# Performance work log

Measured on AMD Instinct MI355X. Metric: run time of the kernel, lower is better.

Reference implementation:

```python
import jax, jax.numpy as jnp
import numpy as np

EMBED = 768
HEAD = 256

def setup_inputs() -> dict:
    key = jax.random.key(0)
    k1, k2, k3, k4 = jax.random.split(key, 4)
    res_stream = jax.random.normal(k1, (512, 128, EMBED), dtype=jnp.float32)
    # torch Linear(embed, head, bias=False): y = x @ W.T, W: [head, embed].
    # Store as [embed, head] so y = x @ W.
    Wk = jax.random.normal(k2, (EMBED, HEAD), dtype=jnp.float32) * (EMBED ** -0.5)
    Wq = jax.random.normal(k3, (EMBED, HEAD), dtype=jnp.float32) * (EMBED ** -0.5)
    Wv = jax.random.normal(k4, (EMBED, HEAD), dtype=jnp.float32) * (EMBED ** -0.5)
    return {"res_stream": res_stream, "Wk": Wk, "Wq": Wq, "Wv": Wv}

def reference(res_stream, Wk, Wq, Wv):
    B, T, E = res_stream.shape
    q = jnp.einsum('bte,eh->bth', res_stream, Wq)  # [B,T,H]
    k = jnp.einsum('bte,eh->bth', res_stream, Wk)
    v = jnp.einsum('bte,eh->bth', res_stream, Wv)
    # NOTE: original scales by embed**-0.5 (not head_size**-0.5)
    scores = jnp.einsum('bth,bsh->bts', q, k) * (E ** -0.5)  # [B,T,T]
    causal = jnp.tril(jnp.ones((T, T), dtype=bool))
    scores = jnp.where(causal, scores, -jnp.inf)
    attn = jax.nn.softmax(scores, axis=-1)
    # dropout: eval mode (identity) for deterministic reference
    return jnp.einsum('bts,bsh->bth', attn, v)  # [B,T,H]
```

## Files before the change

kernel.cpp:

```cpp
#include <hip/hip_runtime.h>
#include <hip/hip_bf16.h>

typedef float f32x4 __attribute__((ext_vector_type(4)));
typedef short bfx8 __attribute__((ext_vector_type(8)));

typedef const __attribute__((address_space(1))) void* gvp;
typedef __attribute__((address_space(3))) void* lvp;

static __device__ __forceinline__ unsigned short f2bf(float f) {
    return __builtin_bit_cast(unsigned short, __float2bfloat16(f));
}

static __device__ __forceinline__ ushort4 cvt4(f32x4 v) {
    return make_ushort4(f2bf(v[0]), f2bf(v[1]), f2bf(v[2]), f2bf(v[3]));
}

__global__ void prep_w(const float* __restrict__ Wk, const float* __restrict__ Wq,
                       const float* __restrict__ Wv, unsigned short* __restrict__ WT) {
    const int n = blockIdx.x;
    const int e = threadIdx.x;
    const int which = n >> 8;
    const int h = n & 255;
    const float* W = (which == 0) ? Wq : (which == 1) ? Wk : Wv;
    WT[(size_t)n * 768 + e] = f2bf(W[(size_t)e * 256 + h]);
}

__global__ __launch_bounds__(256, 2) void qkv_gemm(const float* __restrict__ X,
                                                   const unsigned short* __restrict__ WT,
                                                   unsigned short* __restrict__ QKV) {
    __shared__ unsigned short Ab[2][128][64];
    __shared__ unsigned short Bb[2][128][64];

    const int tid = threadIdx.x;
    const int bid = blockIdx.x;
    const int l   = (bid & 7) * 384 + (bid >> 3);
    const int bn  = l % 6;
    const int bm  = l / 6;
    const int m0 = bm * 128;
    const int n0 = bn * 128;
    const int w = tid >> 6, lane = tid & 63;
    const int wr = w >> 1, wc = w & 1;
    const int lrow = lane & 15, lhi = lane >> 4;
    const bool vswap = (bn >= 4);

    f32x4 acc[4][4];
    const f32x4 zero = {0.f, 0.f, 0.f, 0.f};
#pragma unroll
    for (int i = 0; i < 4; ++i)
#pragma unroll
        for (int j = 0; j < 4; ++j) acc[i][j] = zero;

    f32x4 areg[8];

#define STAGE_A_LOAD(kt)                                                       \
    {                                                                          \
        const int k0s = (kt) * 64;                                             \
        _Pragma("unroll")                                                      \
        for (int i = 0; i < 8; ++i) {                                          \
            const int f = i * 256 + tid;                                       \
            const int row = f >> 4, col = (f & 15) * 4;                        \
            areg[i] = *(const f32x4*)(X + (size_t)(m0 + row) * 768 + k0s + col); \
        }                                                                      \
    }
#define STAGE_A_WRITE(bs)                                                      \
    {                                                                          \
        _Pragma("unroll")                                                      \
        for (int i = 0; i < 8; ++i) {                                          \
            const int f = i * 256 + tid;                                       \
            const int row = f >> 4;                                            \
            const int cb  = (f & 15) * 8;                                      \
            const int cbs = cb ^ ((row & 7) << 4);                             \
            *(ushort4*)((char*)&Ab[bs][0][0] + row * 128 + cbs) = cvt4(areg[i]); \
        }                                                                      \
    }
#define STAGE_B(kt, bs)                                                        \
    {                                                                          \
        const int k0s = (kt) * 64;                                             \
        _Pragma("unroll")                                                      \
        for (int i = 0; i < 4; ++i) {                                          \
            const int f = i * 256 + tid;                                       \
            const int row = f >> 3;                                            \
            const int cb  = (f & 7) * 16;                                      \
            const int cbs = cb ^ ((row & 7) << 4);                             \
            const unsigned short* g = WT + (size_t)(n0 + row) * 768 + k0s + (cbs >> 1); \
            char* lp = (char*)&Bb[bs][0][0] + i * 4096 + w * 1024;             \
            __builtin_amdgcn_global_load_lds((gvp)g, (lvp)lp, 16, 0, 0);       \
        }                                                                      \
    }

    STAGE_B(0, 0);
    STAGE_A_LOAD(0);
    STAGE_A_WRITE(0);
    __syncthreads();

    int cur = 0;
    for (int kt = 0; kt < 12; ++kt) {
        if (kt < 11) {
            STAGE_B(kt + 1, cur ^ 1);
            STAGE_A_LOAD(kt + 1);
        }
#pragma unroll
        for (int kk = 0; kk < 2; ++kk) {
            const int kb2 = (kk * 32 + lhi * 8) * 2;
            bfx8 a[4], bb4[4];
#pragma unroll
            for (int mi = 0; mi < 4; ++mi) {
                const int arow = wr * 64 + mi * 16 + lrow;
                const char* ap = (const char*)&Ab[cur][arow][0];
                a[mi] = *(const bfx8*)(ap + (kb2 ^ ((arow & 7) << 4)));
            }
#pragma unroll
            for (int ni = 0; ni < 4; ++ni) {
                const int brow = wc * 64 + ni * 16 + lrow;
                const char* bp = (const char*)&Bb[cur][brow][0];
                bb4[ni] = *(const bfx8*)(bp + (kb2 ^ ((brow & 7) << 4)));
            }
            if (!vswap) {
#pragma unroll
                for (int mi = 0; mi < 4; ++mi)
#pragma unroll
                    for (int ni = 0; ni < 4; ++ni)
                        acc[mi][ni] = __builtin_amdgcn_mfma_f32_16x16x32_bf16(
                            a[mi], bb4[ni], acc[mi][ni], 0, 0, 0);
            } else {
#pragma unroll
                for (int ni = 0; ni < 4; ++ni)
#pragma unroll
                    for (int mi = 0; mi < 4; ++mi)
                        acc[ni][mi] = __builtin_amdgcn_mfma_f32_16x16x32_bf16(
                            bb4[ni], a[mi], acc[ni][mi], 0, 0, 0);
            }
        }
        if (kt < 11) STAGE_A_WRITE(cur ^ 1);
        __syncthreads();
        cur ^= 1;
    }

    const int b = bm;
    if (!vswap) {
        const int which = bn >> 1;
        const size_t base = ((size_t)(b * 3 + which)) << 15;
        const int hbase = (bn & 1) * 128;
#pragma unroll
        for (int mi = 0; mi < 4; ++mi)
#pragma unroll
            for (int ni = 0; ni < 4; ++ni) {
                const int t = wr * 64 + mi * 16 + lhi * 4;
                const int h = hbase + wc * 64 + ni * 16 + lrow;
#pragma unroll
                for (int j = 0; j < 4; ++j)
                    QKV[base + (size_t)(t + j) * 256 + h] = f2bf(acc[mi][ni][j]);
            }
    } else {
        const size_t base = ((size_t)(b * 3 + 2)) << 15;
#pragma unroll
        for (int ni = 0; ni < 4; ++ni)
#pragma unroll
            for (int mi = 0; mi < 4; ++mi) {
                const int h = (bn - 4) * 128 + wc * 64 + ni * 16 + lhi * 4;
                const int t = wr * 64 + mi * 16 + lrow;
#pragma unroll
                for (int j = 0; j < 4; ++j)
                    QKV[base + (size_t)(h + j) * 128 + t] = f2bf(acc[ni][mi][j]);
            }
    }
}

__global__ __launch_bounds__(512) void attn(const unsigned short* __restrict__ QKV,
                                            float* __restrict__ Out) {
    __shared__ unsigned short Kl[128][264];
    __shared__ unsigned short Vt[256][136];

    const int b = blockIdx.x;
    const int tid = threadIdx.x;
    const int w = tid >> 6, lane = tid & 63;
    const int lrow = lane & 15, lhi = lane >> 4;

    const unsigned short* Qb = QKV + ((size_t)(b * 3 + 0) << 15);
    const unsigned short* Kb = QKV + ((size_t)(b * 3 + 1) << 15);
    const unsigned short* Vb = QKV + ((size_t)(b * 3 + 2) << 15);

    const int t0 = w * 16;
    bfx8 aq[8];
#pragma unroll
    for (int kk = 0; kk < 8; ++kk)
        aq[kk] = *(const bfx8*)(Qb + (size_t)(t0 + lrow) * 256 + kk * 32 + lhi * 8);

#pragma unroll
    for (int i = 0; i < 8; ++i) {
        int f = i * 512 + tid;
        {
            int row = f >> 5, c = (f & 31) * 8;
            *(bfx8*)&Kl[row][c] = *(const bfx8*)(Kb + (size_t)row * 256 + c);
        }
        {
            int row = f >> 4, c = (f & 15) * 8;
            *(bfx8*)&Vt[row][c] = *(const bfx8*)(Vb + (size_t)row * 128 + c);
        }
    }
    __syncthreads();

    f32x4 sacc[8];
    const f32x4 zero = {0.f, 0.f, 0.f, 0.f};
#pragma unroll
    for (int sj = 0; sj < 8; ++sj) sacc[sj] = zero;
#pragma unroll
    for (int kk = 0; kk < 8; ++kk) {
        const int kb = kk * 32 + lhi * 8;
#pragma unroll
        for (int sj = 0; sj < 8; ++sj) {
            bfx8 bk = *(const bfx8*)&Kl[sj * 16 + lrow][kb];
            sacc[sj] = __builtin_amdgcn_mfma_f32_16x16x32_bf16(aq[kk], bk, sacc[sj], 0, 0, 0);
        }
    }

    const float scale = 0.03608439182435161f;
    float inv[4];
#pragma unroll
    for (int j = 0; j < 4; ++j) {
        const int t = t0 + lhi * 4 + j;
        float m = -1e30f;
#pragma unroll
        for (int sj = 0; sj < 8; ++sj) {
            int s = sj * 16 + lrow;
            float vv = sacc[sj][j] * scale;
            vv = (s <= t) ? vv : -1e30f;
            sacc[sj][j] = vv;
            m = fmaxf(m, vv);
        }
#pragma unroll
        for (int d = 1; d < 16; d <<= 1) m = fmaxf(m, __shfl_xor(m, d));
        float sum = 0.f;
#pragma unroll
        for (int sj = 0; sj < 8; ++sj) {
            float e = __expf(sacc[sj][j] - m);
            sacc[sj][j] = e;
            sum += e;
        }
#pragma unroll
        for (int d = 1; d < 16; d <<= 1) sum += __shfl_xor(sum, d);
        inv[j] = 1.0f / sum;
    }

    __syncthreads();

    unsigned short* Pl = &Kl[0][0] + (size_t)w * (16 * 136);
#pragma unroll
    for (int sj = 0; sj < 8; ++sj)
#pragma unroll
        for (int j = 0; j < 4; ++j)
            Pl[(lhi * 4 + j) * 136 + sj * 16 + lrow] = f2bf(sacc[sj][j] * inv[j]);

    bfx8 pa[4];
#pragma unroll
    for (int kk = 0; kk < 4; ++kk)
        pa[kk] = *(const bfx8*)(Pl + lrow * 136 + kk * 32 + lhi * 8);

    f32x4 oacc[16];
#pragma unroll
    for (int ni = 0; ni < 16; ++ni) oacc[ni] = zero;
#pragma unroll
    for (int ni = 0; ni < 16; ++ni) {
#pragma unroll
        for (int kk = 0; kk < 4; ++kk) {
            bfx8 bv = *(const bfx8*)&Vt[ni * 16 + lrow][kk * 32 + lhi * 8];
            oacc[ni] = __builtin_amdgcn_mfma_f32_16x16x32_bf16(pa[kk], bv, oacc[ni], 0, 0, 0);
        }
    }

    float* Ob = Out + (size_t)b * 128 * 256;
#pragma unroll
    for (int ni = 0; ni < 16; ++ni) {
#pragma unroll
        for (int j = 0; j < 4; ++j) {
            const int t = t0 + lhi * 4 + j;
            const int h = ni * 16 + lrow;
            Ob[(size_t)t * 256 + h] = oacc[ni][j];
        }
    }
}

extern "C" void kernel_launch(void* const* d_in, const int* in_sizes, int n_in,
                              void* d_out, int out_size, void* d_ws, size_t ws_size,
                              hipStream_t stream) {
    (void)in_sizes; (void)n_in; (void)out_size; (void)ws_size;
    const float* X  = (const float*)d_in[0];
    const float* Wk = (const float*)d_in[1];
    const float* Wq = (const float*)d_in[2];
    const float* Wv = (const float*)d_in[3];

    unsigned short* WT  = (unsigned short*)d_ws;
    unsigned short* QKV = WT + (size_t)768 * 768;
    float* Out = (float*)d_out;

    prep_w<<<768, 768, 0, stream>>>(Wk, Wq, Wv, WT);
    qkv_gemm<<<3072, 256, 0, stream>>>(X, WT, QKV);
    attn<<<512, 512, 0, stream>>>(QKV, Out);
}
```

Measured before the change: 201.8 us.

## Enlarge QKV GEMM tiles to 256x256 and stage output through LDS

The QKV projection GEMM goes from 128x128 tiles with 4 waves to 256x256 tiles with 8 waves. Each wave now holds a 128x64 accumulator, so per-tile operand reuse goes up and the grid shrinks from 3072 to 768 blocks. The epilogue now writes bf16 results to a swizzled LDS buffer and then does coalesced 16-byte global stores, replacing scattered 2-byte stores; V is still written transposed. In exchange the kernel uses 128KB of LDS and more registers, which lowers occupancy, and there are fewer blocks to cover the 256 CUs.

```diff
diff --git a/kernel.cpp b/kernel.cpp
--- a/kernel.cpp
+++ b/kernel.cpp
@@ -25,28 +25,27 @@
     WT[(size_t)n * 768 + e] = f2bf(W[(size_t)e * 256 + h]);
 }
 
-__global__ __launch_bounds__(256, 2) void qkv_gemm(const float* __restrict__ X,
+__global__ __launch_bounds__(512, 2) void qkv_gemm(const float* __restrict__ X,
                                                    const unsigned short* __restrict__ WT,
                                                    unsigned short* __restrict__ QKV) {
-    __shared__ unsigned short Ab[2][128][64];
-    __shared__ unsigned short Bb[2][128][64];
+    __shared__ __align__(16) char LDS[131072];
 
     const int tid = threadIdx.x;
     const int bid = blockIdx.x;
-    const int l   = (bid & 7) * 384 + (bid >> 3);
-    const int bn  = l % 6;
-    const int bm  = l / 6;
-    const int m0 = bm * 128;
-    const int n0 = bn * 128;
+    const int l   = (bid & 7) * 96 + (bid >> 3);
+    const int bn  = l % 3;
+    const int bm  = l / 3;
+    const int m0 = bm * 256;
+    const int n0 = bn * 256;
     const int w = tid >> 6, lane = tid & 63;
-    const int wr = w >> 1, wc = w & 1;
+    const int wr = w >> 2, wc = w & 3;
     const int lrow = lane & 15, lhi = lane >> 4;
-    const bool vswap = (bn >= 4);
-
-    f32x4 acc[4][4];
+    const bool vswap = (bn == 2);
+
+    f32x4 acc[8][4];
     const f32x4 zero = {0.f, 0.f, 0.f, 0.f};
 #pragma unroll
-    for (int i = 0; i < 4; ++i)
+    for (int i = 0; i < 8; ++i)
 #pragma unroll
         for (int j = 0; j < 4; ++j) acc[i][j] = zero;
 
@@ -57,7 +56,7 @@
         const int k0s = (kt) * 64;                                             \
         _Pragma("unroll")                                                      \
         for (int i = 0; i < 8; ++i) {                                          \
-            const int f = i * 256 + tid;                                       \
+            const int f = i * 512 + tid;                                       \
             const int row = f >> 4, col = (f & 15) * 4;                        \
             areg[i] = *(const f32x4*)(X + (size_t)(m0 + row) * 768 + k0s + col); \
         }                                                                      \
@@ -66,11 +65,11 @@
     {                                                                          \
         _Pragma("unroll")                                                      \
         for (int i = 0; i < 8; ++i) {                                          \
-            const int f = i * 256 + tid;                                       \
+            const int f = i * 512 + tid;                                       \
             const int row = f >> 4;                                            \
             const int cb  = (f & 15) * 8;                                      \
             const int cbs = cb ^ ((row & 7) << 4);                             \
-            *(ushort4*)((char*)&Ab[bs][0][0] + row * 128 + cbs) = cvt4(areg[i]); \
+            *(ushort4*)(LDS + (bs) * 32768 + row * 128 + cbs) = cvt4(areg[i]); \
         }                                                                      \
     }
 #define STAGE_B(kt, bs)                                                        \
@@ -78,12 +77,12 @@
         const int k0s = (kt) * 64;                                             \
         _Pragma("unroll")                                                      \
         for (int i = 0; i < 4; ++i) {                                          \
-            const int f = i * 256 + tid;                                       \
+            const int f = i * 512 + tid;                                       \
             const int row = f >> 3;                                            \
             const int cb  = (f & 7) * 16;                                      \
             const int cbs = cb ^ ((row & 7) << 4);                             \
             const unsigned short* g = WT + (size_t)(n0 + row) * 768 + k0s + (cbs >> 1); \
-            char* lp = (char*)&Bb[bs][0][0] + i * 4096 + w * 1024;             \
+            char* lp = LDS + 65536 + (bs) * 32768 + i * 8192 + w * 1024;       \
             __builtin_amdgcn_global_load_lds((gvp)g, (lvp)lp, 16, 0, 0);       \
         }                                                                      \
     }
@@ -102,33 +101,33 @@
 #pragma unroll
         for (int kk = 0; kk < 2; ++kk) {
             const int kb2 = (kk * 32 + lhi * 8) * 2;
-            bfx8 a[4], bb4[4];
-#pragma unroll
-            for (int mi = 0; mi < 4; ++mi) {
-                const int arow = wr * 64 + mi * 16 + lrow;
-                const char* ap = (const char*)&Ab[cur][arow][0];
-                a[mi] = *(const bfx8*)(ap + (kb2 ^ ((arow & 7) << 4)));
-            }
+            bfx8 a[8], bb4[4];
 #pragma unroll
             for (int ni = 0; ni < 4; ++ni) {
                 const int brow = wc * 64 + ni * 16 + lrow;
-                const char* bp = (const char*)&Bb[cur][brow][0];
-                bb4[ni] = *(const bfx8*)(bp + (kb2 ^ ((brow & 7) << 4)));
+                bb4[ni] = *(const bfx8*)(LDS + 65536 + cur * 32768 + brow * 128 +
+                                         (kb2 ^ ((brow & 7) << 4)));
+            }
+#pragma unroll
+            for (int mi = 0; mi < 8; ++mi) {
+                const int arow = wr * 128 + mi * 16 + lrow;
+                a[mi] = *(const bfx8*)(LDS + cur * 32768 + arow * 128 +
+                                       (kb2 ^ ((arow & 7) << 4)));
             }
             if (!vswap) {
 #pragma unroll
-                for (int mi = 0; mi < 4; ++mi)
+                for (int mi = 0; mi < 8; ++mi)
 #pragma unroll
                     for (int ni = 0; ni < 4; ++ni)
                         acc[mi][ni] = __builtin_amdgcn_mfma_f32_16x16x32_bf16(
                             a[mi], bb4[ni], acc[mi][ni], 0, 0, 0);
             } else {
 #pragma unroll
-                for (int ni = 0; ni < 4; ++ni)
-#pragma unroll
-                    for (int mi = 0; mi < 4; ++mi)
-                        acc[ni][mi] = __builtin_amdgcn_mfma_f32_16x16x32_bf16(
-                            bb4[ni], a[mi], acc[ni][mi], 0, 0, 0);
+                for (int mi = 0; mi < 8; ++mi)
+#pragma unroll
+                    for (int ni = 0; ni < 4; ++ni)
+                        acc[mi][ni] = __builtin_amdgcn_mfma_f32_16x16x32_bf16(
+                            bb4[ni], a[mi], acc[mi][ni], 0, 0, 0);
             }
         }
         if (kt < 11) STAGE_A_WRITE(cur ^ 1);
@@ -136,33 +135,52 @@
         cur ^= 1;
     }
 
-    const int b = bm;
     if (!vswap) {
-        const int which = bn >> 1;
-        const size_t base = ((size_t)(b * 3 + which)) << 15;
-        const int hbase = (bn & 1) * 128;
-#pragma unroll
-        for (int mi = 0; mi < 4; ++mi)
+#pragma unroll
+        for (int mi = 0; mi < 8; ++mi)
 #pragma unroll
             for (int ni = 0; ni < 4; ++ni) {
-                const int t = wr * 64 + mi * 16 + lhi * 4;
-                const int h = hbase + wc * 64 + ni * 16 + lrow;
-#pragma unroll
-                for (int j = 0; j < 4; ++j)
-                    QKV[base + (size_t)(t + j) * 256 + h] = f2bf(acc[mi][ni][j]);
+                const int h2 = (wc * 64 + ni * 16 + lrow) * 2;
+#pragma unroll
+                for (int j = 0; j < 4; ++j) {
+                    const int trel = wr * 128 + mi * 16 + lhi * 4 + j;
+                    *(unsigned short*)(LDS + trel * 512 + (h2 ^ ((trel & 7) << 4))) =
+                        f2bf(acc[mi][ni][j]);
+                }
             }
     } else {
-        const size_t base = ((size_t)(b * 3 + 2)) << 15;
-#pragma unroll
-        for (int ni = 0; ni < 4; ++ni)
-#pragma unroll
-            for (int mi = 0; mi < 4; ++mi) {
-                const int h = (bn - 4) * 128 + wc * 64 + ni * 16 + lhi * 4;
-                const int t = wr * 64 + mi * 16 + lrow;
-#pragma unroll
-                for (int j = 0; j < 4; ++j)
-                    QKV[base + (size_t)(h + j) * 128 + t] = f2bf(acc[ni][mi][j]);
-            }
+#pragma unroll
+        for (int mi = 0; mi < 8; ++mi)
+#pragma unroll
+            for (int ni = 0; ni < 4; ++ni) {
+                const int t2 = (wr * 128 + mi * 16 + lrow) * 2;
+#pragma unroll
+                for (int j = 0; j < 4; ++j) {
+                    const int h = wc * 64 + ni * 16 + lhi * 4 + j;
+                    *(unsigned short*)(LDS + h * 512 + (t2 ^ ((h & 7) << 4))) =
+                        f2bf(acc[mi][ni][j]);
+                }
+            }
+    }
+    __syncthreads();
+
+#pragma unroll
+    for (int i = 0; i < 16; ++i) {
+        const int f = i * 512 + tid;
+        const int r  = f >> 5;
+        const int c8 = (f & 31) * 8;
+        const bfx8 v = *(const bfx8*)(LDS + r * 512 + ((c8 * 2) ^ ((r & 7) << 4)));
+        if (bn < 2) {
+            const int b = bm * 2 + (r >> 7);
+            unsigned short* g = QKV + (((size_t)(b * 3 + bn)) << 15) +
+                                (size_t)(r & 127) * 256 + c8;
+            *(bfx8*)g = v;
+        } else {
+            const int b = bm * 2 + (c8 >> 7);
+            unsigned short* g = QKV + (((size_t)(b * 3 + 2)) << 15) +
+                                (size_t)r * 128 + (c8 & 127);
+            *(bfx8*)g = v;
+        }
     }
 }
 
@@ -294,6 +312,6 @@
     float* Out = (float*)d_out;
 
     prep_w<<<768, 768, 0, stream>>>(Wk, Wq, Wv, WT);
-    qkv_gemm<<<3072, 256, 0, stream>>>(X, WT, QKV);
+    qkv_gemm<<<768, 512, 0, stream>>>(X, WT, QKV);
     attn<<<512, 512, 0, stream>>>(QKV, Out);
 }
```

Result: slower. 741.4 us (+267.4%).
